# Kernel tuning notes

Measured on AMD Instinct MI355X. Metric: run time of the kernel, lower is better.

## Reference

```python
import jax, jax.numpy as jnp
import numpy as np

H = 1024
F = 1024


def _lstm_cell(x, h, c, Wih, Whh, b):
    # PyTorch gate order: i, f, g, o
    gates = x @ Wih.T + h @ Whh.T + b
    i, f, g, o = jnp.split(gates, 4, axis=-1)
    c = jax.nn.sigmoid(f) * c + jax.nn.sigmoid(i) * jnp.tanh(g)
    h = jax.nn.sigmoid(o) * jnp.tanh(c)
    return h, c


def setup_inputs() -> dict:
    key = jax.random.key(0)
    ks = iter(jax.random.split(key, 32))
    def rn(shape, s=0.05):
        return (s * jax.random.normal(next(ks), shape)).astype(jnp.float32)
    return {
        "tsn_feat_seq": rn((4096, F), 1.0),
        "W_fe": rn((H, F)), "b_fe": rn((H,)),
        "gW_ih0": rn((4 * H, 2 * H)), "gW_ihR": rn((4, 4 * H, H)),
        "gW_hh": rn((5, 4 * H, H)), "gb_ih": rn((5, 4 * H)), "gb_hh": rn((5, 4 * H)),
        "rW_ih": rn((4 * H, 2 * H)), "rW_hh": rn((4 * H, H)),
        "rb_ih": rn((4 * H,)), "rb_hh": rn((4 * H,)),
        "Wp": rn((H, 3 * H)), "bp": rn((H,)),
        "We2a": rn((2513, H)), "be2a": rn((2513,)),
        "We2v": rn((125, H)), "be2v": rn((125,)),
        "We2n": rn((352, H)), "be2n": rn((352,)),
    }


def reference(tsn_feat_seq, W_fe, b_fe, gW_ih0, gW_ihR, gW_hh, gb_ih, gb_hh,
              rW_ih, rW_hh, rb_ih, rb_hh, Wp, bp,
              We2a, be2a, We2v, be2v, We2n, be2n):
    # feat embedding of max-pooled TSN features (batch is always 1 after max)
    fs = jnp.max(tsn_feat_seq, axis=0) @ W_fe.T + b_fe          # [H]
    cur_action = (fs @ We2a.T + be2a)[None, :]                   # [1, 2513]

    # 5-layer goal LSTM, single time step, zero initial states;
    # input = concat(feat_state, zero action_state)
    z = jnp.zeros(H, fs.dtype)
    x = jnp.concatenate([fs, z])                                 # [2H]
    h, _ = _lstm_cell(x, z, z, gW_ih0, gW_hh[0], gb_ih[0] + gb_hh[0])
    for k in range(4):
        h, _ = _lstm_cell(h, z, z, gW_ihR[k], gW_hh[k + 1], gb_ih[k + 1] + gb_hh[k + 1])
    g = h                                                        # goal_state [H]

    rb = rb_ih + rb_hh

    def expand(a_in, f_in, best_d, best_f):
        # 10 single-layer LSTM steps with FIXED input (as in the source loop)
        xin = jnp.concatenate([a_in, f_in])                      # [2H]
        def rnn_step(carry, _):
            hh, cc = carry
            hh, cc = _lstm_cell(xin, hh, cc, rW_ih, rW_hh, rb)
            return (hh, cc), hh
        _, a_js = jax.lax.scan(rnn_step, (z, z), None, length=10)   # [10, H]
        # featpredictor: relu(Linear(concat(feat, action, goal))); dropout = eval identity
        pf = jnp.concatenate([jnp.broadcast_to(f_in, (10, H)), a_js,
                              jnp.broadcast_to(g, (10, H))], axis=1)  # [10, 3H]
        nfs = jax.nn.relu(pf @ Wp.T + bp)                        # [10, H]
        # sequential greedy best-feat update defines the scores (order matters)
        def score_step(carry, nf):
            bd, bf = carry
            d = jnp.sum((nf - g) ** 2) / H
            s = bd - d
            upd = d < bd
            return (jnp.where(upd, d, bd), jnp.where(upd, nf, bf)), s
        (bd, bf), scores = jax.lax.scan(score_step, (best_d, best_f), nfs)
        return a_js, nfs, scores, bd, bf

    # expansion 1: root node (action=0, feat=fs); best_feat_state starts at fs
    bd0 = jnp.sum((fs - g) ** 2) / H
    a1, f1, s1, bd1, bf1 = expand(z, fs, bd0, fs)
    # priority queue pops lowest score -> expansion 2 from that node
    i_star = jnp.argmin(s1)
    a2in = a1[i_star]
    f2in = f1[i_star]
    a2, f2, s2, _, _ = expand(a2in, f2in, bd1, bf1)

    # chain means: exp1 chain = [root, child]; exp2 chain = [root, n2, child]
    am = jnp.concatenate([a1 / 2.0, (a2in + a2) / 3.0], axis=0)        # [20, H]
    fm = jnp.concatenate([(fs + f1) / 2.0, (fs + f2in + f2) / 3.0], axis=0)
    scores = jnp.concatenate([s1.at[i_star].set(jnp.inf), s2])          # popped node removed
    _, idx = jax.lax.top_k(-scores, 2)                                  # 2 lowest scores, ascending
    pa = am[idx]                                                        # [2, H]
    pfeat = fm[idx]                                                     # [2, H]
    pgoal = jnp.broadcast_to(g, (2, H))

    pred_actions = pa @ We2a.T + be2a                                   # [2, 2513]
    pred_verbs = pa @ We2v.T + be2v                                     # [2, 125]
    pred_nouns = pa @ We2n.T + be2n                                     # [2, 352]
    # returned feat_state is the feat of the last popped (expanded) node
    return (pred_actions, pred_verbs, pred_nouns, pfeat, pgoal, f2in[None, :], cur_action)
```

## Files before the change

### kernel.cpp

```cpp
#include <hip/hip_runtime.h>
#include <math.h>


__device__ __forceinline__ float sigf(float x) { return 1.0f / (1.0f + expf(-x)); }

__device__ __forceinline__ float wave_red(float v) {
#pragma unroll
    for (int s = 32; s; s >>= 1) v += __shfl_down(v, s, 64);
    return v;
}

__device__ __forceinline__ float dotf(const float* __restrict__ w,
                                      const float* __restrict__ x, int lane) {
    float acc = 0.f;
#pragma unroll
    for (int j = 0; j < 4; ++j) {
        float4 a = *reinterpret_cast<const float4*>(w + j * 256 + lane * 4);
        float4 b = *reinterpret_cast<const float4*>(x + j * 256 + lane * 4);
        acc += a.x * b.x + a.y * b.y + a.z * b.z + a.w * b.w;
    }
    return acc;
}

__global__ void colmax_part_k(const float* __restrict__ tsn, float* __restrict__ part) {
    int tid = threadIdx.x;
    const float4* t4 = reinterpret_cast<const float4*>(tsn);
    float4 m = make_float4(-INFINITY, -INFINITY, -INFINITY, -INFINITY);
    int r0 = blockIdx.x * 512;
    for (int r = r0; r < r0 + 512; ++r) {
        float4 v = t4[(size_t)r * 256 + tid];
        m.x = fmaxf(m.x, v.x); m.y = fmaxf(m.y, v.y);
        m.z = fmaxf(m.z, v.z); m.w = fmaxf(m.w, v.w);
    }
    reinterpret_cast<float4*>(part + (size_t)blockIdx.x * 1024)[tid] = m;
}
__global__ void colmax_fin_k(const float* __restrict__ part, float* __restrict__ maxv) {
    int c = blockIdx.x * 256 + threadIdx.x;
    float m = -INFINITY;
    for (int b = 0; b < 8; ++b) m = fmaxf(m, part[b * 1024 + c]);
    maxv[c] = m;
}

__global__ void gemv_k(const float* __restrict__ W, int ld, int nrows,
                       const float* __restrict__ xA, int offA,
                       const float* __restrict__ xB, int offB,
                       const float* __restrict__ b1,
                       const float* __restrict__ b2,
                       float* __restrict__ yF, float* __restrict__ yOut) {
    int wave = threadIdx.x >> 6, lane = threadIdx.x & 63;
    int row = blockIdx.x * 4 + wave;
    if (row >= nrows) return;
    const float* wr = W + (size_t)row * ld;
    float acc = 0.f;
    if (xA) acc += dotf(wr + offA, xA, lane);
    if (xB) acc += dotf(wr + offB, xB, lane);
    acc = wave_red(acc);
    if (lane == 0) {
        if (b1) acc += b1[row];
        if (b2) acc += b2[row];
        if (yF) yF[row] = acc;
        if (yOut) yOut[row] = acc;
    }
}

__global__ void lstm_fused_k(const float* __restrict__ W, int ld, int off,
                             const float* __restrict__ x,
                             const float* __restrict__ b1,
                             const float* __restrict__ b2,
                             const float* __restrict__ gx,
                             const float* __restrict__ cc_in,
                             float* __restrict__ cc_out,
                             float* __restrict__ h_out) {
    __shared__ float glds[4][4];
    int wave = threadIdx.x >> 6, lane = threadIdx.x & 63;
    int j0 = blockIdx.x * 4;
#pragma unroll
    for (int jj = 0; jj < 4; ++jj) {
        int row = wave * 1024 + j0 + jj;
        float acc = dotf(W + (size_t)row * ld + off, x, lane);
        acc = wave_red(acc);
        if (lane == 0) {
            if (b1) acc += b1[row];
            if (b2) acc += b2[row];
            if (gx) acc += gx[row];
            glds[wave][jj] = acc;
        }
    }
    __syncthreads();
    if (threadIdx.x < 4) {
        int jj = threadIdx.x, j = j0 + jj;
        float gi = glds[0][jj], gf = glds[1][jj], gg = glds[2][jj], go = glds[3][jj];
        float c = sigf(gi) * tanhf(gg);
        if (cc_in) c += sigf(gf) * cc_in[j];
        float h = sigf(go) * tanhf(c);
        if (cc_out) cc_out[j] = c;
        h_out[j] = h;
    }
}

__global__ void cell0_k(const float* __restrict__ gx, float* __restrict__ cc_out,
                        float* __restrict__ h_out) {
    int j = blockIdx.x * 256 + threadIdx.x;
    float gi = gx[j], gg = gx[2048 + j], go = gx[3072 + j];
    float c = sigf(gi) * tanhf(gg);
    float h = sigf(go) * tanhf(c);
    cc_out[j] = c;
    h_out[j] = h;
}

__global__ void nfs_k(const float* __restrict__ Wp, const float* __restrict__ ajs,
                      const float* __restrict__ sv, float* __restrict__ nfs) {
    int wave = threadIdx.x >> 6, lane = threadIdx.x & 63;
    int i = blockIdx.x * 4 + wave;
    const float* wr = Wp + (size_t)i * 3072 + 1024;
    float wf[16];
#pragma unroll
    for (int j = 0; j < 4; ++j) {
        float4 a = *reinterpret_cast<const float4*>(wr + j * 256 + lane * 4);
        wf[j * 4 + 0] = a.x; wf[j * 4 + 1] = a.y; wf[j * 4 + 2] = a.z; wf[j * 4 + 3] = a.w;
    }
    float acc[10];
#pragma unroll
    for (int t = 0; t < 10; ++t) acc[t] = 0.f;
#pragma unroll
    for (int t = 0; t < 10; ++t) {
        const float* a = ajs + t * 1024;
#pragma unroll
        for (int j = 0; j < 4; ++j) {
            float4 b = *reinterpret_cast<const float4*>(a + j * 256 + lane * 4);
            acc[t] += wf[j * 4 + 0] * b.x + wf[j * 4 + 1] * b.y +
                      wf[j * 4 + 2] * b.z + wf[j * 4 + 3] * b.w;
        }
    }
#pragma unroll
    for (int t = 0; t < 10; ++t) {
        float r = wave_red(acc[t]);
        if (lane == 0) nfs[t * 1024 + i] = fmaxf(sv[i] + r, 0.f);
    }
}

__global__ void scores1_k(const float* __restrict__ nfs1, const float* __restrict__ g,
                          const float* __restrict__ fs, const float* __restrict__ ajs1,
                          float* __restrict__ s1, float* __restrict__ bd1_out,
                          int* __restrict__ istar_out, float* __restrict__ a2in,
                          float* __restrict__ f2in, float* __restrict__ out_f2in) {
    __shared__ float red[256];
    __shared__ float d[11];
    __shared__ int istar_sh;
    int tid = threadIdx.x;
    for (int t = 0; t < 11; ++t) {
        const float* v = (t < 10) ? (nfs1 + t * 1024) : fs;
        float p = 0.f;
        for (int j = tid * 4; j < tid * 4 + 4; ++j) { float df = v[j] - g[j]; p += df * df; }
        red[tid] = p; __syncthreads();
        for (int s = 128; s; s >>= 1) { if (tid < s) red[tid] += red[tid + s]; __syncthreads(); }
        if (tid == 0) d[t] = red[0] * (1.0f / 1024.0f);
        __syncthreads();
    }
    if (tid == 0) {
        float bd = d[10];
        float smin = INFINITY; int im = 0;
        for (int t = 0; t < 10; ++t) {
            float s = bd - d[t];
            s1[t] = s;
            if (s < smin) { smin = s; im = t; }
            if (d[t] < bd) bd = d[t];
        }
        *bd1_out = bd; *istar_out = im; istar_sh = im;
    }
    __syncthreads();
    int im = istar_sh;
    for (int j = tid; j < 1024; j += 256) {
        float a = ajs1[im * 1024 + j], f = nfs1[im * 1024 + j];
        a2in[j] = a; f2in[j] = f; out_f2in[j] = f;
    }
}

__global__ void scores2_k(const float* __restrict__ nfs2, const float* __restrict__ g,
                          const float* __restrict__ fs, const float* __restrict__ ajs1,
                          const float* __restrict__ nfs1, const float* __restrict__ ajs2,
                          const float* __restrict__ a2in, const float* __restrict__ f2in,
                          const float* __restrict__ s1, const float* __restrict__ bd1,
                          const int* __restrict__ istar, float* __restrict__ pa,
                          float* __restrict__ out) {
    __shared__ float red[256];
    __shared__ float d[10];
    __shared__ int sel[2];
    int tid = threadIdx.x;
    for (int t = 0; t < 10; ++t) {
        const float* v = nfs2 + t * 1024;
        float p = 0.f;
        for (int j = tid * 4; j < tid * 4 + 4; ++j) { float df = v[j] - g[j]; p += df * df; }
        red[tid] = p; __syncthreads();
        for (int s = 128; s; s >>= 1) { if (tid < s) red[tid] += red[tid + s]; __syncthreads(); }
        if (tid == 0) d[t] = red[0] * (1.0f / 1024.0f);
        __syncthreads();
    }
    if (tid == 0) {
        float sc[20];
        int im = *istar;
        for (int t = 0; t < 10; ++t) sc[t] = (t == im) ? INFINITY : s1[t];
        float bd = *bd1;
        for (int t = 0; t < 10; ++t) {
            float s = bd - d[t];
            sc[10 + t] = s;
            if (d[t] < bd) bd = d[t];
        }
        int i0 = 0; float m0 = INFINITY;
        for (int t = 0; t < 20; ++t) if (sc[t] < m0) { m0 = sc[t]; i0 = t; }
        int i1 = 0; float m1 = INFINITY;
        for (int t = 0; t < 20; ++t) { if (t == i0) continue; if (sc[t] < m1) { m1 = sc[t]; i1 = t; } }
        sel[0] = i0; sel[1] = i1;
    }
    __syncthreads();
    for (int p = 0; p < 2; ++p) {
        int idx = sel[p];
        for (int j = tid; j < 1024; j += 256) {
            float av, fv;
            if (idx < 10) {
                av = ajs1[idx * 1024 + j] * 0.5f;
                fv = (fs[j] + nfs1[idx * 1024 + j]) * 0.5f;
            } else {
                int t = idx - 10;
                av = (a2in[j] + ajs2[t * 1024 + j]) * (1.0f / 3.0f);
                fv = (fs[j] + f2in[j] + nfs2[t * 1024 + j]) * (1.0f / 3.0f);
            }
            pa[p * 1024 + j] = av;
            out[5980 + p * 1024 + j] = fv;
            out[8028 + p * 1024 + j] = g[j];
        }
    }
}

__global__ void heads_k(const float* __restrict__ We2a, const float* __restrict__ be2a,
                        const float* __restrict__ We2v, const float* __restrict__ be2v,
                        const float* __restrict__ We2n, const float* __restrict__ be2n,
                        const float* __restrict__ pa, float* __restrict__ out) {
    int wave = threadIdx.x >> 6, lane = threadIdx.x & 63;
    int task = blockIdx.x * 4 + wave;
    if (task >= 5980) return;
    int p = (task < 2990) ? 0 : 1;
    int r = task - p * 2990;
    const float* W; const float* b; int outoff, rr;
    if (r < 2513)      { W = We2a; b = be2a; rr = r;        outoff = p * 2513 + rr; }
    else if (r < 2638) { W = We2v; b = be2v; rr = r - 2513; outoff = 5026 + p * 125 + rr; }
    else               { W = We2n; b = be2n; rr = r - 2638; outoff = 5276 + p * 352 + rr; }
    float acc = dotf(W + (size_t)rr * 1024, pa + p * 1024, lane);
    acc = wave_red(acc);
    if (lane == 0) out[outoff] = acc + b[rr];
}

extern "C" void kernel_launch(void* const* d_in, const int* in_sizes, int n_in,
                              void* d_out, int out_size, void* d_ws, size_t ws_size,
                              hipStream_t stream) {
    const float* tsn    = (const float*)d_in[0];
    const float* W_fe   = (const float*)d_in[1];
    const float* b_fe   = (const float*)d_in[2];
    const float* gW_ih0 = (const float*)d_in[3];
    const float* gW_ihR = (const float*)d_in[4];
    const float* gb_ih  = (const float*)d_in[6];
    const float* gb_hh  = (const float*)d_in[7];
    const float* rW_ih  = (const float*)d_in[8];
    const float* rW_hh  = (const float*)d_in[9];
    const float* rb_ih  = (const float*)d_in[10];
    const float* rb_hh  = (const float*)d_in[11];
    const float* Wp     = (const float*)d_in[12];
    const float* bp     = (const float*)d_in[13];
    const float* We2a   = (const float*)d_in[14];
    const float* be2a   = (const float*)d_in[15];
    const float* We2v   = (const float*)d_in[16];
    const float* be2v   = (const float*)d_in[17];
    const float* We2n   = (const float*)d_in[18];
    const float* be2n   = (const float*)d_in[19];
    float* out = (float*)d_out;

    float* w = (float*)d_ws;
    float* part  = w + 0;
    float* maxv  = w + 8192;
    float* fs    = w + 9216;
    float* hgA   = w + 10240;
    float* hgB   = w + 11264;
    float* gx    = w + 12288;
    float* ajs1  = w + 16384;
    float* nfs1  = w + 26624;
    float* ajs2  = w + 36864;
    float* nfs2  = w + 47104;
    float* cc0   = w + 57344;
    float* cc1   = w + 58368;
    float* sv    = w + 59392;
    float* a2in  = w + 60416;
    float* f2in  = w + 61440;
    float* pa    = w + 62464;
    float* s1    = w + 64512;
    float* bd1   = w + 64524;
    int*   istar = (int*)(w + 64528);

    colmax_part_k<<<8, 256, 0, stream>>>(tsn, part);
    colmax_fin_k<<<4, 256, 0, stream>>>(part, maxv);
    gemv_k<<<256, 256, 0, stream>>>(W_fe, 1024, 1024, maxv, 0, nullptr, 0, b_fe, nullptr, fs, nullptr);
    gemv_k<<<629, 256, 0, stream>>>(We2a, 1024, 2513, fs, 0, nullptr, 0, be2a, nullptr, nullptr, out + 11100);

    lstm_fused_k<<<256, 256, 0, stream>>>(gW_ih0, 2048, 0, fs, gb_ih, gb_hh, nullptr, nullptr, nullptr, hgA);
    lstm_fused_k<<<256, 256, 0, stream>>>(gW_ihR + (size_t)0 * 4194304, 1024, 0, hgA, gb_ih + 1 * 4096, gb_hh + 1 * 4096, nullptr, nullptr, nullptr, hgB);
    lstm_fused_k<<<256, 256, 0, stream>>>(gW_ihR + (size_t)1 * 4194304, 1024, 0, hgB, gb_ih + 2 * 4096, gb_hh + 2 * 4096, nullptr, nullptr, nullptr, hgA);
    lstm_fused_k<<<256, 256, 0, stream>>>(gW_ihR + (size_t)2 * 4194304, 1024, 0, hgA, gb_ih + 3 * 4096, gb_hh + 3 * 4096, nullptr, nullptr, nullptr, hgB);
    lstm_fused_k<<<256, 256, 0, stream>>>(gW_ihR + (size_t)3 * 4194304, 1024, 0, hgB, gb_ih + 4 * 4096, gb_hh + 4 * 4096, nullptr, nullptr, nullptr, hgA);
    float* g = hgA;

    gemv_k<<<1024, 256, 0, stream>>>(rW_ih, 2048, 4096, nullptr, 0, fs, 1024, rb_ih, rb_hh, gx, nullptr);
    cell0_k<<<4, 256, 0, stream>>>(gx, cc0, ajs1);
    for (int t = 1; t < 10; ++t) {
        float* cin = ((t - 1) & 1) ? cc1 : cc0;
        float* cout = (t & 1) ? cc1 : cc0;
        lstm_fused_k<<<256, 256, 0, stream>>>(rW_hh, 1024, 0, ajs1 + (t - 1) * 1024,
                                              nullptr, nullptr, gx, cin, cout, ajs1 + t * 1024);
    }
    gemv_k<<<256, 256, 0, stream>>>(Wp, 3072, 1024, fs, 0, g, 2048, bp, nullptr, sv, nullptr);
    nfs_k<<<256, 256, 0, stream>>>(Wp, ajs1, sv, nfs1);
    scores1_k<<<1, 256, 0, stream>>>(nfs1, g, fs, ajs1, s1, bd1, istar, a2in, f2in, out + 10076);

    gemv_k<<<1024, 256, 0, stream>>>(rW_ih, 2048, 4096, a2in, 0, f2in, 1024, rb_ih, rb_hh, gx, nullptr);
    cell0_k<<<4, 256, 0, stream>>>(gx, cc0, ajs2);
    for (int t = 1; t < 10; ++t) {
        float* cin = ((t - 1) & 1) ? cc1 : cc0;
        float* cout = (t & 1) ? cc1 : cc0;
        lstm_fused_k<<<256, 256, 0, stream>>>(rW_hh, 1024, 0, ajs2 + (t - 1) * 1024,
                                              nullptr, nullptr, gx, cin, cout, ajs2 + t * 1024);
    }
    gemv_k<<<256, 256, 0, stream>>>(Wp, 3072, 1024, f2in, 0, g, 2048, bp, nullptr, sv, nullptr);
    nfs_k<<<256, 256, 0, stream>>>(Wp, ajs2, sv, nfs2);
    scores2_k<<<1, 256, 0, stream>>>(nfs2, g, fs, ajs1, nfs1, ajs2, a2in, f2in, s1, bd1, istar, pa, out);

    heads_k<<<1495, 256, 0, stream>>>(We2a, be2a, We2v, be2v, We2n, be2n, pa, out);
}
```

Baseline: 500.2 us.

## Widen colmax and LSTM parallelism, fuse gate cells, sv, and output heads

The column max is split across 256 blocks instead of 8, with a 4-way unrolled load loop. The LSTM kernel now gives each hidden unit its own 512-thread block, with two waves per gate splitting the dot product. The input-projection step is folded into that kernel and writes gx, which removes the separate cell0 kernel. The sv projection is fused into nfs_k, and the heads kernel computes both prediction rows plus the cur_action row from one weight read. Together these aim to raise occupancy and memory parallelism and cut launches and repeated weight reads, at the cost of a larger workspace and a single-thread epilogue per block.

```diff
diff --git a/kernel.cpp b/kernel.cpp
--- a/kernel.cpp
+++ b/kernel.cpp
@@ -26,97 +26,94 @@
     int tid = threadIdx.x;
     const float4* t4 = reinterpret_cast<const float4*>(tsn);
     float4 m = make_float4(-INFINITY, -INFINITY, -INFINITY, -INFINITY);
-    int r0 = blockIdx.x * 512;
-    for (int r = r0; r < r0 + 512; ++r) {
-        float4 v = t4[(size_t)r * 256 + tid];
-        m.x = fmaxf(m.x, v.x); m.y = fmaxf(m.y, v.y);
-        m.z = fmaxf(m.z, v.z); m.w = fmaxf(m.w, v.w);
+    int r0 = blockIdx.x * 16;
+    for (int r = r0; r < r0 + 16; r += 4) {
+        float4 v0 = t4[(size_t)(r + 0) * 256 + tid];
+        float4 v1 = t4[(size_t)(r + 1) * 256 + tid];
+        float4 v2 = t4[(size_t)(r + 2) * 256 + tid];
+        float4 v3 = t4[(size_t)(r + 3) * 256 + tid];
+        m.x = fmaxf(fmaxf(m.x, v0.x), fmaxf(v1.x, fmaxf(v2.x, v3.x)));
+        m.y = fmaxf(fmaxf(m.y, v0.y), fmaxf(v1.y, fmaxf(v2.y, v3.y)));
+        m.z = fmaxf(fmaxf(m.z, v0.z), fmaxf(v1.z, fmaxf(v2.z, v3.z)));
+        m.w = fmaxf(fmaxf(m.w, v0.w), fmaxf(v1.w, fmaxf(v2.w, v3.w)));
     }
     reinterpret_cast<float4*>(part + (size_t)blockIdx.x * 1024)[tid] = m;
 }
 __global__ void colmax_fin_k(const float* __restrict__ part, float* __restrict__ maxv) {
     int c = blockIdx.x * 256 + threadIdx.x;
     float m = -INFINITY;
-    for (int b = 0; b < 8; ++b) m = fmaxf(m, part[b * 1024 + c]);
+    for (int b = 0; b < 256; ++b) m = fmaxf(m, part[b * 1024 + c]);
     maxv[c] = m;
 }
 
 __global__ void gemv_k(const float* __restrict__ W, int ld, int nrows,
-                       const float* __restrict__ xA, int offA,
-                       const float* __restrict__ xB, int offB,
+                       const float* __restrict__ xA,
                        const float* __restrict__ b1,
-                       const float* __restrict__ b2,
-                       float* __restrict__ yF, float* __restrict__ yOut) {
+                       float* __restrict__ yF) {
     int wave = threadIdx.x >> 6, lane = threadIdx.x & 63;
     int row = blockIdx.x * 4 + wave;
     if (row >= nrows) return;
-    const float* wr = W + (size_t)row * ld;
+    float acc = dotf(W + (size_t)row * ld, xA, lane);
+    acc = wave_red(acc);
+    if (lane == 0) yF[row] = acc + b1[row];
+}
+
+__global__ __launch_bounds__(512) void lstm_step_k(
+    const float* __restrict__ W, int ld, int off, int nr,
+    const float* __restrict__ x,
+    const float* __restrict__ b1, const float* __restrict__ b2,
+    const float* __restrict__ gxIn, float* __restrict__ gxOut,
+    const float* __restrict__ cc_in, float* __restrict__ cc_out,
+    float* __restrict__ h_out) {
+    __shared__ float part[8];
+    int tid = threadIdx.x;
+    int w = tid >> 6, lane = tid & 63;
+    int gate = w >> 1, half = w & 1;
+    int j = blockIdx.x;
+    int row = gate * 1024 + j;
+    int halflen = nr * 256;
+    const float* wr = W + (size_t)row * ld + off + half * halflen;
+    const float* xr = x + half * halflen;
     float acc = 0.f;
-    if (xA) acc += dotf(wr + offA, xA, lane);
-    if (xB) acc += dotf(wr + offB, xB, lane);
+    for (int r = 0; r < nr; ++r) {
+        float4 a = *reinterpret_cast<const float4*>(wr + r * 256 + lane * 4);
+        float4 b = *reinterpret_cast<const float4*>(xr + r * 256 + lane * 4);
+        acc += a.x * b.x + a.y * b.y + a.z * b.z + a.w * b.w;
+    }
     acc = wave_red(acc);
-    if (lane == 0) {
-        if (b1) acc += b1[row];
-        if (b2) acc += b2[row];
-        if (yF) yF[row] = acc;
-        if (yOut) yOut[row] = acc;
-    }
-}
-
-__global__ void lstm_fused_k(const float* __restrict__ W, int ld, int off,
-                             const float* __restrict__ x,
-                             const float* __restrict__ b1,
-                             const float* __restrict__ b2,
-                             const float* __restrict__ gx,
-                             const float* __restrict__ cc_in,
-                             float* __restrict__ cc_out,
-                             float* __restrict__ h_out) {
-    __shared__ float glds[4][4];
-    int wave = threadIdx.x >> 6, lane = threadIdx.x & 63;
-    int j0 = blockIdx.x * 4;
-#pragma unroll
-    for (int jj = 0; jj < 4; ++jj) {
-        int row = wave * 1024 + j0 + jj;
-        float acc = dotf(W + (size_t)row * ld + off, x, lane);
-        acc = wave_red(acc);
-        if (lane == 0) {
-            if (b1) acc += b1[row];
-            if (b2) acc += b2[row];
-            if (gx) acc += gx[row];
-            glds[wave][jj] = acc;
-        }
-    }
+    if (lane == 0) part[w] = acc;
     __syncthreads();
-    if (threadIdx.x < 4) {
-        int jj = threadIdx.x, j = j0 + jj;
-        float gi = glds[0][jj], gf = glds[1][jj], gg = glds[2][jj], go = glds[3][jj];
-        float c = sigf(gi) * tanhf(gg);
-        if (cc_in) c += sigf(gf) * cc_in[j];
-        float h = sigf(go) * tanhf(c);
+    if (tid == 0) {
+        float g4[4];
+#pragma unroll
+        for (int gi = 0; gi < 4; ++gi) {
+            int rw = gi * 1024 + j;
+            float v = part[2 * gi] + part[2 * gi + 1];
+            if (b1) v += b1[rw];
+            if (b2) v += b2[rw];
+            if (gxIn) v += gxIn[rw];
+            if (gxOut) gxOut[rw] = v;
+            g4[gi] = v;
+        }
+        float c = sigf(g4[0]) * tanhf(g4[2]);
+        if (cc_in) c += sigf(g4[1]) * cc_in[j];
+        float h = sigf(g4[3]) * tanhf(c);
         if (cc_out) cc_out[j] = c;
         h_out[j] = h;
     }
 }
 
-__global__ void cell0_k(const float* __restrict__ gx, float* __restrict__ cc_out,
-                        float* __restrict__ h_out) {
-    int j = blockIdx.x * 256 + threadIdx.x;
-    float gi = gx[j], gg = gx[2048 + j], go = gx[3072 + j];
-    float c = sigf(gi) * tanhf(gg);
-    float h = sigf(go) * tanhf(c);
-    cc_out[j] = c;
-    h_out[j] = h;
-}
-
-__global__ void nfs_k(const float* __restrict__ Wp, const float* __restrict__ ajs,
-                      const float* __restrict__ sv, float* __restrict__ nfs) {
+__global__ void nfs_sv_k(const float* __restrict__ Wp, const float* __restrict__ f_in,
+                         const float* __restrict__ g, const float* __restrict__ bp,
+                         const float* __restrict__ ajs, float* __restrict__ nfs) {
     int wave = threadIdx.x >> 6, lane = threadIdx.x & 63;
     int i = blockIdx.x * 4 + wave;
-    const float* wr = Wp + (size_t)i * 3072 + 1024;
+    const float* wr = Wp + (size_t)i * 3072;
+    float svacc = dotf(wr, f_in, lane) + dotf(wr + 2048, g, lane);
     float wf[16];
 #pragma unroll
     for (int j = 0; j < 4; ++j) {
-        float4 a = *reinterpret_cast<const float4*>(wr + j * 256 + lane * 4);
+        float4 a = *reinterpret_cast<const float4*>(wr + 1024 + j * 256 + lane * 4);
         wf[j * 4 + 0] = a.x; wf[j * 4 + 1] = a.y; wf[j * 4 + 2] = a.z; wf[j * 4 + 3] = a.w;
     }
     float acc[10];
@@ -132,10 +129,11 @@
                       wf[j * 4 + 2] * b.z + wf[j * 4 + 3] * b.w;
         }
     }
+    float svr = wave_red(svacc);
 #pragma unroll
     for (int t = 0; t < 10; ++t) {
         float r = wave_red(acc[t]);
-        if (lane == 0) nfs[t * 1024 + i] = fmaxf(sv[i] + r, 0.f);
+        if (lane == 0) nfs[t * 1024 + i] = fmaxf(svr + bp[i] + r, 0.f);
     }
 }
 
@@ -235,19 +233,35 @@
 __global__ void heads_k(const float* __restrict__ We2a, const float* __restrict__ be2a,
                         const float* __restrict__ We2v, const float* __restrict__ be2v,
                         const float* __restrict__ We2n, const float* __restrict__ be2n,
-                        const float* __restrict__ pa, float* __restrict__ out) {
+                        const float* __restrict__ fs, const float* __restrict__ pa,
+                        float* __restrict__ out) {
     int wave = threadIdx.x >> 6, lane = threadIdx.x & 63;
     int task = blockIdx.x * 4 + wave;
-    if (task >= 5980) return;
-    int p = (task < 2990) ? 0 : 1;
-    int r = task - p * 2990;
-    const float* W; const float* b; int outoff, rr;
-    if (r < 2513)      { W = We2a; b = be2a; rr = r;        outoff = p * 2513 + rr; }
-    else if (r < 2638) { W = We2v; b = be2v; rr = r - 2513; outoff = 5026 + p * 125 + rr; }
-    else               { W = We2n; b = be2n; rr = r - 2638; outoff = 5276 + p * 352 + rr; }
-    float acc = dotf(W + (size_t)rr * 1024, pa + p * 1024, lane);
-    acc = wave_red(acc);
-    if (lane == 0) out[outoff] = acc + b[rr];
+    if (task >= 2990) return;
+    const float* W; const float* b; int rr, o0, o1, o2; bool doFs;
+    if (task < 2513)      { W = We2a; b = be2a; rr = task;        o0 = rr;        o1 = 2513 + rr; o2 = 11100 + rr; doFs = true; }
+    else if (task < 2638) { W = We2v; b = be2v; rr = task - 2513; o0 = 5026 + rr; o1 = 5151 + rr; o2 = 0; doFs = false; }
+    else                  { W = We2n; b = be2n; rr = task - 2638; o0 = 5276 + rr; o1 = 5628 + rr; o2 = 0; doFs = false; }
+    const float* wr = W + (size_t)rr * 1024;
+    float a0 = 0.f, a1 = 0.f, a2 = 0.f;
+#pragma unroll
+    for (int r = 0; r < 4; ++r) {
+        int base = r * 256 + lane * 4;
+        float4 wv = *reinterpret_cast<const float4*>(wr + base);
+        float4 p0 = *reinterpret_cast<const float4*>(pa + base);
+        float4 p1 = *reinterpret_cast<const float4*>(pa + 1024 + base);
+        float4 fv = *reinterpret_cast<const float4*>(fs + base);
+        a0 += wv.x * p0.x + wv.y * p0.y + wv.z * p0.z + wv.w * p0.w;
+        a1 += wv.x * p1.x + wv.y * p1.y + wv.z * p1.z + wv.w * p1.w;
+        a2 += wv.x * fv.x + wv.y * fv.y + wv.z * fv.z + wv.w * fv.w;
+    }
+    a0 = wave_red(a0); a1 = wave_red(a1); a2 = wave_red(a2);
+    if (lane == 0) {
+        float bb = b[rr];
+        out[o0] = a0 + bb;
+        out[o1] = a1 + bb;
+        if (doFs) out[o2] = a2 + bb;
+    }
 }
 
 extern "C" void kernel_launch(void* const* d_in, const int* in_sizes, int n_in,
@@ -276,60 +290,62 @@
 
     float* w = (float*)d_ws;
     float* part  = w + 0;
-    float* maxv  = w + 8192;
-    float* fs    = w + 9216;
-    float* hgA   = w + 10240;
-    float* hgB   = w + 11264;
-    float* gx    = w + 12288;
-    float* ajs1  = w + 16384;
-    float* nfs1  = w + 26624;
-    float* ajs2  = w + 36864;
-    float* nfs2  = w + 47104;
-    float* cc0   = w + 57344;
-    float* cc1   = w + 58368;
-    float* sv    = w + 59392;
-    float* a2in  = w + 60416;
-    float* f2in  = w + 61440;
-    float* pa    = w + 62464;
-    float* s1    = w + 64512;
-    float* bd1   = w + 64524;
-    int*   istar = (int*)(w + 64528);
-
-    colmax_part_k<<<8, 256, 0, stream>>>(tsn, part);
+    float* maxv  = w + 262144;
+    float* fs    = w + 263168;
+    float* hgA   = w + 264192;
+    float* hgB   = w + 265216;
+    float* gx    = w + 266240;
+    float* ajs1  = w + 270336;
+    float* nfs1  = w + 280576;
+    float* ajs2  = w + 290816;
+    float* nfs2  = w + 301056;
+    float* cc0   = w + 311296;
+    float* cc1   = w + 312320;
+    float* xin2  = w + 313344;
+    float* a2in  = xin2;
+    float* f2in  = xin2 + 1024;
+    float* pa    = w + 315392;
+    float* s1    = w + 317440;
+    float* bd1   = w + 317456;
+    int*   istar = (int*)(w + 317460);
+
+    colmax_part_k<<<256, 256, 0, stream>>>(tsn, part);
     colmax_fin_k<<<4, 256, 0, stream>>>(part, maxv);
-    gemv_k<<<256, 256, 0, stream>>>(W_fe, 1024, 1024, maxv, 0, nullptr, 0, b_fe, nullptr, fs, nullptr);
-    gemv_k<<<629, 256, 0, stream>>>(We2a, 1024, 2513, fs, 0, nullptr, 0, be2a, nullptr, nullptr, out + 11100);
-
-    lstm_fused_k<<<256, 256, 0, stream>>>(gW_ih0, 2048, 0, fs, gb_ih, gb_hh, nullptr, nullptr, nullptr, hgA);
-    lstm_fused_k<<<256, 256, 0, stream>>>(gW_ihR + (size_t)0 * 4194304, 1024, 0, hgA, gb_ih + 1 * 4096, gb_hh + 1 * 4096, nullptr, nullptr, nullptr, hgB);
-    lstm_fused_k<<<256, 256, 0, stream>>>(gW_ihR + (size_t)1 * 4194304, 1024, 0, hgB, gb_ih + 2 * 4096, gb_hh + 2 * 4096, nullptr, nullptr, nullptr, hgA);
-    lstm_fused_k<<<256, 256, 0, stream>>>(gW_ihR + (size_t)2 * 4194304, 1024, 0, hgA, gb_ih + 3 * 4096, gb_hh + 3 * 4096, nullptr, nullptr, nullptr, hgB);
-    lstm_fused_k<<<256, 256, 0, stream>>>(gW_ihR + (size_t)3 * 4194304, 1024, 0, hgB, gb_ih + 4 * 4096, gb_hh + 4 * 4096, nullptr, nullptr, nullptr, hgA);
+    gemv_k<<<256, 256, 0, stream>>>(W_fe, 1024, 1024, maxv, b_fe, fs);
+
+    lstm_step_k<<<1024, 512, 0, stream>>>(gW_ih0, 2048, 0, 2, fs, gb_ih, gb_hh,
+                                          nullptr, nullptr, nullptr, nullptr, hgA);
+    lstm_step_k<<<1024, 512, 0, stream>>>(gW_ihR + (size_t)0 * 4194304, 1024, 0, 2, hgA,
+                                          gb_ih + 4096, gb_hh + 4096, nullptr, nullptr, nullptr, nullptr, hgB);
+    lstm_step_k<<<1024, 512, 0, stream>>>(gW_ihR + (size_t)1 * 4194304, 1024, 0, 2, hgB,
+                                          gb_ih + 8192, gb_hh + 8192, nullptr, nullptr, nullptr, nullptr, hgA);
+    lstm_step_k<<<1024, 512, 0, stream>>>(gW_ihR + (size_t)2 * 4194304, 1024, 0, 2, hgA,
+                                          gb_ih + 12288, gb_hh + 12288, nullptr, nullptr, nullptr, nullptr, hgB);
+    lstm_step_k<<<1024, 512, 0, stream>>>(gW_ihR + (size_t)3 * 4194304, 1024, 0, 2, hgB,
+                                          gb_ih + 16384, gb_hh + 16384, nullptr, nullptr, nullptr, nullptr, hgA);
     float* g = hgA;
 
-    gemv_k<<<1024, 256, 0, stream>>>(rW_ih, 2048, 4096, nullptr, 0, fs, 1024, rb_ih, rb_hh, gx, nullptr);
-    cell0_k<<<4, 256, 0, stream>>>(gx, cc0, ajs1);
+    lstm_step_k<<<1024, 512, 0, stream>>>(rW_ih, 2048, 1024, 2, fs, rb_ih, rb_hh,
+                                          nullptr, gx, nullptr, cc0, ajs1);
     for (int t = 1; t < 10; ++t) {
         float* cin = ((t - 1) & 1) ? cc1 : cc0;
         float* cout = (t & 1) ? cc1 : cc0;
-        lstm_fused_k<<<256, 256, 0, stream>>>(rW_hh, 1024, 0, ajs1 + (t - 1) * 1024,
-                                              nullptr, nullptr, gx, cin, cout, ajs1 + t * 1024);
-    }
-    gemv_k<<<256, 256, 0, stream>>>(Wp, 3072, 1024, fs, 0, g, 2048, bp, nullptr, sv, nullptr);
-    nfs_k<<<256, 256, 0, stream>>>(Wp, ajs1, sv, nfs1);
+        lstm_step_k<<<1024, 512, 0, stream>>>(rW_hh, 1024, 0, 2, ajs1 + (t - 1) * 1024,
+                                              nullptr, nullptr, gx, nullptr, cin, cout, ajs1 + t * 1024);
+    }
+    nfs_sv_k<<<256, 256, 0, stream>>>(Wp, fs, g, bp, ajs1, nfs1);
     scores1_k<<<1, 256, 0, stream>>>(nfs1, g, fs, ajs1, s1, bd1, istar, a2in, f2in, out + 10076);
 
-    gemv_k<<<1024, 256, 0, stream>>>(rW_ih, 2048, 4096, a2in, 0, f2in, 1024, rb_ih, rb_hh, gx, nullptr);
-    cell0_k<<<4, 256, 0, stream>>>(gx, cc0, ajs2);
+    lstm_step_k<<<1024, 512, 0, stream>>>(rW_ih, 2048, 0, 4, xin2, rb_ih, rb_hh,
+                                          nullptr, gx, nullptr, cc0, ajs2);
     for (int t = 1; t < 10; ++t) {
         float* cin = ((t - 1) & 1) ? cc1 : cc0;
         float* cout = (t & 1) ? cc1 : cc0;
-        lstm_fused_k<<<256, 256, 0, stream>>>(rW_hh, 1024, 0, ajs2 + (t - 1) * 1024,
-                                              nullptr, nullptr, gx, cin, cout, ajs2 + t * 1024);
-    }
-    gemv_k<<<256, 256, 0, stream>>>(Wp, 3072, 1024, f2in, 0, g, 2048, bp, nullptr, sv, nullptr);
-    nfs_k<<<256, 256, 0, stream>>>(Wp, ajs2, sv, nfs2);
+        lstm_step_k<<<1024, 512, 0, stream>>>(rW_hh, 1024, 0, 2, ajs2 + (t - 1) * 1024,
+                                              nullptr, nullptr, gx, nullptr, cin, cout, ajs2 + t * 1024);
+    }
+    nfs_sv_k<<<256, 256, 0, stream>>>(Wp, f2in, g, bp, ajs2, nfs2);
     scores2_k<<<1, 256, 0, stream>>>(nfs2, g, fs, ajs1, nfs1, ajs2, a2in, f2in, s1, bd1, istar, pa, out);
 
-    heads_k<<<1495, 256, 0, stream>>>(We2a, be2a, We2v, be2v, We2n, be2n, pa, out);
-}
+    heads_k<<<748, 256, 0, stream>>>(We2a, be2a, We2v, be2v, We2n, be2n, fs, pa, out);
+}
```

Result: no change. 500.9 us (+0.1%).
